# Kernel optimization log

Hardware: AMD Instinct MI355X
Metric: run time of the kernel (lower is better)

Reference implementation:

```python
import jax, jax.numpy as jnp
import numpy as np

N_EMBD = 1024
N_HEAD = 16
HEAD_SIZE = N_EMBD // N_HEAD


def setup_inputs() -> dict:
    key = jax.random.key(0)
    k_x, k_w, k_b = jax.random.split(key, 3)
    B, T, C = 2, 2048, N_EMBD
    x = jax.random.normal(k_x, (B, T, C), dtype=jnp.float32)
    # Linear(n_embd, 3*n_embd): weight [C, 3C] (applied as x @ W), bias [3C]
    w_qkv = jax.random.normal(k_w, (C, 3 * C), dtype=jnp.float32) * (1.0 / np.sqrt(C))
    b_qkv = jax.random.normal(k_b, (3 * C,), dtype=jnp.float32) * 0.02
    return {"x": x, "w_qkv": w_qkv, "b_qkv": b_qkv}


def reference(x, w_qkv, b_qkv):
    B, T, C = x.shape
    H, D = N_HEAD, HEAD_SIZE
    qkv = x @ w_qkv + b_qkv                      # [B, T, 3C]
    q, k, v = jnp.split(qkv, 3, axis=-1)         # each [B, T, C]
    # [B, T, C] -> [B, H, T, D]
    q = q.reshape(B, T, H, D).transpose(0, 2, 1, 3)
    k = k.reshape(B, T, H, D).transpose(0, 2, 1, 3)
    v = v.reshape(B, T, H, D).transpose(0, 2, 1, 3)
    scores = jnp.einsum('bhqd,bhkd->bhqk', q, k) / jnp.sqrt(jnp.float32(D))
    causal = jnp.tril(jnp.ones((T, T), dtype=bool))  # allow j <= i
    scores = jnp.where(causal[None, None, :, :], scores, -jnp.inf)
    weights = jax.nn.softmax(scores, axis=-1)    # [B, H, T, T]
    out = jnp.einsum('bhqk,bhkd->bhqd', weights, v)
    out = out.transpose(0, 2, 1, 3).reshape(B, T, C)
    return out
```

## Files before the change

### kernel.cpp

```cpp
#include <hip/hip_runtime.h>
#include <hip/hip_bf16.h>


#define CDIM  1024
#define C3    3072
#define HS    64
#define TLEN  2048
#define KVT   64
#define KSTR  72
#define VSTR  72
#define SCL   0.1803368801111204f

typedef __attribute__((ext_vector_type(8))) short bf16x8;
typedef __attribute__((ext_vector_type(4))) float f32x4;
typedef __attribute__((ext_vector_type(4))) unsigned short u16x4;

__device__ __forceinline__ unsigned short f2b(float f) {
    unsigned u = __float_as_uint(f);
    unsigned r = (u + 0x7FFFu + ((u >> 16) & 1u)) >> 16;
    return (unsigned short)r;
}
__device__ __forceinline__ float b2f(unsigned short u) {
    return __uint_as_float(((unsigned)u) << 16);
}
__device__ __forceinline__ float fexp2(float x) {
    return __builtin_amdgcn_exp2f(x);
}
__device__ __forceinline__ unsigned pkbf(float a, float b) {
    float2 f; f.x = a; f.y = b;
    __hip_bfloat162 h = __float22bfloat162_rn(f);
    union { __hip_bfloat162 h2; unsigned u; } c;
    c.h2 = h;
    return c.u;
}
__device__ __forceinline__ void gl_lds16(const unsigned short* g, unsigned short* l) {
    __builtin_amdgcn_global_load_lds((const __attribute__((address_space(1))) void*)g,
                                     (__attribute__((address_space(3))) void*)l, 16, 0, 0);
}
__device__ __forceinline__ int detect_bf(const void* bias, int lane) {
    unsigned w = ((const unsigned*)bias)[lane];
    unsigned e = (w >> 7) & 0xFF;
    unsigned long long m = __ballot(e >= 100 && e <= 135);
    return __popcll(m) >= 48;
}

__device__ __forceinline__ void plswap(unsigned x, unsigned& y0, unsigned& y1) {
    unsigned aa = x, bb = x;
    asm("v_permlane32_swap_b32 %0, %1" : "+v"(aa), "+v"(bb));
    asm("v_permlane16_swap_b32 %0, %1" : "+v"(aa), "+v"(bb));
    y0 = aa; y1 = bb;
}
__device__ __forceinline__ bf16x8 xfrag(unsigned x00, unsigned x01,
                                        unsigned x10, unsigned x11, int qsel) {
    unsigned y000, y100, y001, y101, y010, y110, y011, y111;
    plswap(x00, y000, y100);
    plswap(x01, y001, y101);
    plswap(x10, y010, y110);
    plswap(x11, y011, y111);
    union { unsigned u[4]; bf16x8 v; } r;
    r.u[0] = qsel ? y010 : y000;
    r.u[1] = qsel ? y011 : y001;
    r.u[2] = qsel ? y110 : y100;
    r.u[3] = qsel ? y111 : y101;
    return r.v;
}

__global__ __launch_bounds__(256) void k_prep(const void* __restrict__ w,
                                              const void* __restrict__ x,
                                              const void* __restrict__ bias,
                                              unsigned short* __restrict__ wt,
                                              unsigned short* __restrict__ xb) {
    __shared__ unsigned short tile[64 * 66];
    int t = threadIdx.x;
    int isbf = detect_bf(bias, t & 63);
    int bid = blockIdx.x;

    if (bid < 768) {
        int n0 = (bid % 48) * 64;
        int k0 = (bid / 48) * 64;
        for (int i = 0; i < 16; ++i) {
            int idx = t + i * 256;
            int r = idx >> 6, c = idx & 63;
            unsigned short v;
            if (isbf) v = ((const unsigned short*)w)[(k0 + r) * C3 + n0 + c];
            else      v = f2b(((const float*)w)[(k0 + r) * C3 + n0 + c]);
            tile[r * 66 + c] = v;
        }
        __syncthreads();
        for (int i = 0; i < 16; ++i) {
            int idx = t + i * 256;
            int r = idx >> 6, c = idx & 63;
            wt[(n0 + r) * CDIM + k0 + c] = tile[c * 66 + r];
        }
    }
    if (!isbf) {
        const float* s = (const float*)x;
        unsigned* d = (unsigned*)xb;
        int base = bid * 1024;
        for (int j = t; j < 1024; j += 256) {
            int idx = base + j;
            float a = s[2 * idx], b = s[2 * idx + 1];
            d[idx] = (unsigned)f2b(a) | ((unsigned)f2b(b) << 16);
        }
    }
}

__global__ __launch_bounds__(256, 3) void k_gemm_qkv(const void* __restrict__ xraw,
                                                     const unsigned short* __restrict__ xb,
                                                     const void* __restrict__ biasraw,
                                                     const unsigned short* __restrict__ Bt,
                                                     unsigned short* __restrict__ qk,
                                                     unsigned short* __restrict__ vtg) {
    __shared__ __align__(16) unsigned short As[128 * 64];
    __shared__ __align__(16) unsigned short Bs[128 * 64];
    int tid  = threadIdx.x;
    int lane = tid & 63, wv = tid >> 6;
    int quad = lane >> 4, l16 = lane & 15;
    int isbf = detect_bf(biasraw, lane);
    const unsigned short* A = isbf ? (const unsigned short*)xraw : xb;

    int m0 = blockIdx.y * 128, n0 = blockIdx.x * 128;
    int wm = (wv >> 1) * 64, wn = (wv & 1) * 64;

    f32x4 acc[4][4] = {};

    int srow = wv * 8 + (lane >> 3);
    int kcg8 = (((lane & 7) ^ (lane >> 3)) * 8);
    const unsigned short* Ag = A  + (m0 + srow) * CDIM + kcg8;
    const unsigned short* Bg = Bt + (n0 + srow) * CDIM + kcg8;
    unsigned short* lA = &As[srow * 64 + (lane & 7) * 8];
    unsigned short* lB = &Bs[srow * 64 + (lane & 7) * 8];

    for (int k0 = 0; k0 < CDIM; k0 += 64) {
        __syncthreads();
        for (int j = 0; j < 4; ++j) {
            gl_lds16(Ag + j * (32 * CDIM), lA + j * (32 * 64));
            gl_lds16(Bg + j * (32 * CDIM), lB + j * (32 * 64));
        }
        Ag += 64; Bg += 64;
        __syncthreads();

        for (int kk = 0; kk < 2; ++kk) {
            int sw = (l16 & 7);
            bf16x8 af[4], bfr[4];
            for (int mt = 0; mt < 4; ++mt)
                af[mt] = *(const bf16x8*)&As[(wm + mt * 16 + l16) * 64 + (((kk * 4 + quad) ^ sw) * 8)];
            for (int nt = 0; nt < 4; ++nt)
                bfr[nt] = *(const bf16x8*)&Bs[(wn + nt * 16 + l16) * 64 + (((kk * 4 + quad) ^ sw) * 8)];
            for (int mt = 0; mt < 4; ++mt)
                for (int nt = 0; nt < 4; ++nt)
                    acc[mt][nt] = __builtin_amdgcn_mfma_f32_16x16x32_bf16(af[mt], bfr[nt], acc[mt][nt], 0, 0, 0);
        }
    }

    if (n0 < 2048) {
        for (int mt = 0; mt < 4; ++mt) {
            int row = m0 + wm + mt * 16 + quad * 4;
            for (int nt = 0; nt < 4; ++nt) {
                int col = n0 + wn + nt * 16 + l16;
                float bv = isbf ? b2f(((const unsigned short*)biasraw)[col])
                                : ((const float*)biasraw)[col];
                for (int i = 0; i < 4; ++i)
                    qk[(row + i) * 2048 + col] = f2b(acc[mt][nt][i] + bv);
            }
        }
    } else {
        for (int mt = 0; mt < 4; ++mt) {
            int row = m0 + wm + mt * 16 + quad * 4;
            int t = row & 2047, b = row >> 11;
            for (int nt = 0; nt < 4; ++nt) {
                int col = n0 + wn + nt * 16 + l16;
                float bv = isbf ? b2f(((const unsigned short*)biasraw)[col])
                                : ((const float*)biasraw)[col];
                int hh = (col - 2048) >> 6, d = (col - 2048) & 63;
                u16x4 pk;
                for (int i = 0; i < 4; ++i) pk[i] = f2b(acc[mt][nt][i] + bv);
                *(u16x4*)&vtg[((b * 16 + hh) * 64 + d) * TLEN + t] = pk;
            }
        }
    }
}

__global__ __launch_bounds__(256, 4) void k_attn(const unsigned short* __restrict__ qk,
                                                 const unsigned short* __restrict__ vtg,
                                                 const void* __restrict__ biasraw,
                                                 void* __restrict__ outv) {
    __shared__ __align__(16) unsigned short Ks[2][64 * KSTR];
    __shared__ __align__(16) unsigned short Vt[2][64 * VSTR];

    int tid  = threadIdx.x;
    int lane = tid & 63, wv = tid >> 6;
    int quad = lane >> 4, l16 = lane & 15;
    int isbf = detect_bf(biasraw, lane);
    int bh = blockIdx.x;
    int g  = 31 - blockIdx.y;
    int b = bh >> 4, h = bh & 15;
    int rowbase = b * TLEN;

    int s_ = wv >> 1;
    int p  = wv & 1;
    int qbase = 64 * g + 32 * s_;
    int T = g + 1;

    bf16x8 qf[2][2];
    for (int qt = 0; qt < 2; ++qt)
        for (int kh = 0; kh < 2; ++kh)
            qf[qt][kh] = *(const bf16x8*)&qk[(rowbase + qbase + qt * 16 + l16) * 2048
                                            + h * HS + kh * 32 + quad * 8];

    f32x4 o[2][4] = {};
    float ls[2] = {0.f, 0.f};

    int srow = tid >> 2;
    int sc   = (tid & 3) * 8;
    const unsigned short* kgB = qk  + (rowbase + srow) * 2048 + CDIM + h * HS + sc;
    const unsigned short* vgB = vtg + (bh * 64 + srow) * TLEN + sc;

    {
        uint4 k0 = *(const uint4*)kgB;
        uint4 k1 = *(const uint4*)(kgB + 32);
        uint4 v0 = *(const uint4*)vgB;
        uint4 v1 = *(const uint4*)(vgB + 32);
        *(uint4*)&Ks[0][srow * KSTR + sc]      = k0;
        *(uint4*)&Ks[0][srow * KSTR + sc + 32] = k1;
        *(uint4*)&Vt[0][srow * VSTR + sc]      = v0;
        *(uint4*)&Vt[0][srow * VSTR + sc + 32] = v1;
    }
    __syncthreads();

    for (int t = 0; t < T; ++t) {
        int cur = t & 1;
        const unsigned short* KsC = Ks[cur];
        const unsigned short* VtC = Vt[cur];
        int kv0 = t * KVT;
        bool act = (p == 0) || (s_ == 1) || (t < T - 1);
        bool dm  = (t == T - 1) && (p == s_);

        uint4 kn0, kn1, vn0, vn1;
        bool pf = (t + 1 < T);
        if (pf) {
            const unsigned short* kg = kgB + (t + 1) * KVT * 2048;
            const unsigned short* vg = vgB + (t + 1) * KVT;
            kn0 = *(const uint4*)kg;
            kn1 = *(const uint4*)(kg + 32);
            vn0 = *(const uint4*)vg;
            vn1 = *(const uint4*)(vg + 32);
        }

        unsigned sp[2][2][2];
        if (act) {
            bf16x8 kf[2][2];
            #pragma unroll
            for (int nt = 0; nt < 2; ++nt) {
                const unsigned short* kb = &KsC[(32 * p + nt * 16 + l16) * KSTR + quad * 8];
                kf[nt][0] = *(const bf16x8*)kb;
                kf[nt][1] = *(const bf16x8*)(kb + 32);
            }
            f32x4 sv[2][2];
            __builtin_amdgcn_s_setprio(1);
            #pragma unroll
            for (int qt = 0; qt < 2; ++qt)
                #pragma unroll
                for (int nt = 0; nt < 2; ++nt) {
                    f32x4 z = {};
                    z = __builtin_amdgcn_mfma_f32_16x16x32_bf16(kf[nt][0], qf[qt][0], z, 0, 0, 0);
                    z = __builtin_amdgcn_mfma_f32_16x16x32_bf16(kf[nt][1], qf[qt][1], z, 0, 0, 0);
                    sv[qt][nt] = z;
                }
            __builtin_amdgcn_s_setprio(0);
            #pragma unroll
            for (int qt = 0; qt < 2; ++qt) {
                float psum = 0.f;
                int q = qbase + qt * 16 + l16;
                #pragma unroll
                for (int nt = 0; nt < 2; ++nt) {
                    float pv[4];
                    #pragma unroll
                    for (int i = 0; i < 4; ++i) {
                        float arg = fminf(fmaf(sv[qt][nt][i], SCL, -12.0f), 30.0f);
                        if (dm) {
                            int kv = kv0 + 32 * p + nt * 16 + quad * 4 + i;
                            if (kv > q) arg = -1e30f;
                        }
                        pv[i] = fexp2(arg);
                        psum += pv[i];
                    }
                    sp[qt][nt][0] = pkbf(pv[0], pv[1]);
                    sp[qt][nt][1] = pkbf(pv[2], pv[3]);
                }
                ls[qt] += psum;
            }
        }

        if (pf) {
            int nxt = cur ^ 1;
            *(uint4*)&Ks[nxt][srow * KSTR + sc]      = kn0;
            *(uint4*)&Ks[nxt][srow * KSTR + sc + 32] = kn1;
            *(uint4*)&Vt[nxt][srow * VSTR + sc]      = vn0;
            *(uint4*)&Vt[nxt][srow * VSTR + sc + 32] = vn1;
        }

        if (act) {
            int qsel = quad & 2;
            bf16x8 f0 = xfrag(sp[0][0][0], sp[0][0][1], sp[0][1][0], sp[0][1][1], qsel);
            bf16x8 f1 = xfrag(sp[1][0][0], sp[1][0][1], sp[1][1][0], sp[1][1][1], qsel);
            __builtin_amdgcn_s_setprio(1);
            #pragma unroll
            for (int dt = 0; dt < 4; ++dt) {
                bf16x8 av = *(const bf16x8*)&VtC[(dt * 16 + l16) * VSTR + 32 * p + quad * 8];
                o[0][dt] = __builtin_amdgcn_mfma_f32_16x16x32_bf16(av, f0, o[0][dt], 0, 0, 0);
                o[1][dt] = __builtin_amdgcn_mfma_f32_16x16x32_bf16(av, f1, o[1][dt], 0, 0, 0);
            }
            __builtin_amdgcn_s_setprio(0);
        }

        __syncthreads();
    }

    #pragma unroll
    for (int qt = 0; qt < 2; ++qt) {
        ls[qt] += __shfl_xor(ls[qt], 16);
        ls[qt] += __shfl_xor(ls[qt], 32);
    }
    float* mrg  = (float*)&Ks[0][0];
    float* lbuf = (float*)&Vt[0][0];

    if (p == 1) {
        #pragma unroll
        for (int qt = 0; qt < 2; ++qt)
            #pragma unroll
            for (int dt = 0; dt < 4; ++dt)
                *(f32x4*)&mrg[s_ * (32 * 68) + (qt * 16 + l16) * 68 + dt * 16 + quad * 4] = o[qt][dt];
        if (quad == 0) {
            lbuf[s_ * 32 + l16]      = ls[0];
            lbuf[s_ * 32 + 16 + l16] = ls[1];
        }
    }
    __syncthreads();
    if (p == 0) {
        #pragma unroll
        for (int qt = 0; qt < 2; ++qt) {
            float lt = ls[qt] + lbuf[s_ * 32 + qt * 16 + l16];
            float inv = 1.0f / lt;
            int q = qbase + qt * 16 + l16;
            if (isbf) {
                unsigned short* out = (unsigned short*)outv;
                #pragma unroll
                for (int dt = 0; dt < 4; ++dt) {
                    f32x4 m = *(const f32x4*)&mrg[s_ * (32 * 68) + (qt * 16 + l16) * 68 + dt * 16 + quad * 4];
                    u16x4 ov;
                    #pragma unroll
                    for (int i = 0; i < 4; ++i) ov[i] = f2b((o[qt][dt][i] + m[i]) * inv);
                    *(u16x4*)&out[(rowbase + q) * CDIM + h * HS + dt * 16 + quad * 4] = ov;
                }
            } else {
                float* out = (float*)outv;
                #pragma unroll
                for (int dt = 0; dt < 4; ++dt) {
                    f32x4 m = *(const f32x4*)&mrg[s_ * (32 * 68) + (qt * 16 + l16) * 68 + dt * 16 + quad * 4];
                    float4 ov;
                    ov.x = (o[qt][dt][0] + m[0]) * inv;
                    ov.y = (o[qt][dt][1] + m[1]) * inv;
                    ov.z = (o[qt][dt][2] + m[2]) * inv;
                    ov.w = (o[qt][dt][3] + m[3]) * inv;
                    *(float4*)&out[(rowbase + q) * CDIM + h * HS + dt * 16 + quad * 4] = ov;
                }
            }
        }
    }
}

extern "C" void kernel_launch(void* const* d_in, const int* in_sizes, int n_in,
                              void* d_out, int out_size, void* d_ws, size_t ws_size,
                              hipStream_t stream) {
    const void* x    = d_in[0];
    const void* w    = d_in[1];
    const void* bias = d_in[2];

    char* ws = (char*)d_ws;
    unsigned short* xb  = (unsigned short*)ws;
    unsigned short* wt  = (unsigned short*)(ws + (8u  << 20));
    unsigned short* qk  = (unsigned short*)(ws + (16u << 20));
    unsigned short* vtg = (unsigned short*)(ws + (32u << 20));

    k_prep<<<2048, 256, 0, stream>>>(w, x, bias, wt, xb);
    k_gemm_qkv<<<dim3(24, 32), 256, 0, stream>>>(x, xb, bias, wt, qk, vtg);
    k_attn<<<dim3(32, 32), 256, 0, stream>>>(qk, vtg, bias, d_out);
}
```

Before: 151.0 us.

## Single-buffer attention K/V tiles for higher occupancy and swizzle GEMM block order

The attention kernel drops double-buffered LDS for K/V to a single buffer. It adds a second barrier per tile so the prefetched registers are written only after all waves finish reading, and raises launch bounds to 6 blocks per CU. The QKV GEMM remaps block indices with a grouped swizzle to improve L2 reuse of weight and activation tiles. The trade is an extra barrier per KV tile and less overlap of LDS writes with compute, in exchange for more resident waves; the merge buffer offsets are recomputed for the smaller shared array.

```diff
diff --git a/kernel.cpp b/kernel.cpp
--- a/kernel.cpp
+++ b/kernel.cpp
@@ -119,7 +119,9 @@
     int isbf = detect_bf(biasraw, lane);
     const unsigned short* A = isbf ? (const unsigned short*)xraw : xb;
 
-    int m0 = blockIdx.y * 128, n0 = blockIdx.x * 128;
+    int lin = blockIdx.x + 24 * blockIdx.y;
+    int swz = (lin & 7) * 96 + (lin >> 3);
+    int m0 = (swz / 24) * 128, n0 = (swz % 24) * 128;
     int wm = (wv >> 1) * 64, wn = (wv & 1) * 64;
 
     f32x4 acc[4][4] = {};
@@ -181,12 +183,13 @@
     }
 }
 
-__global__ __launch_bounds__(256, 4) void k_attn(const unsigned short* __restrict__ qk,
+__global__ __launch_bounds__(256, 6) void k_attn(const unsigned short* __restrict__ qk,
                                                  const unsigned short* __restrict__ vtg,
                                                  const void* __restrict__ biasraw,
                                                  void* __restrict__ outv) {
-    __shared__ __align__(16) unsigned short Ks[2][64 * KSTR];
-    __shared__ __align__(16) unsigned short Vt[2][64 * VSTR];
+    __shared__ __align__(16) unsigned short SM[2 * 64 * KSTR];
+    unsigned short* Ks = SM;
+    unsigned short* Vt = SM + 64 * KSTR;
 
     int tid  = threadIdx.x;
     int lane = tid & 63, wv = tid >> 6;
@@ -221,17 +224,16 @@
         uint4 k1 = *(const uint4*)(kgB + 32);
         uint4 v0 = *(const uint4*)vgB;
         uint4 v1 = *(const uint4*)(vgB + 32);
-        *(uint4*)&Ks[0][srow * KSTR + sc]      = k0;
-        *(uint4*)&Ks[0][srow * KSTR + sc + 32] = k1;
-        *(uint4*)&Vt[0][srow * VSTR + sc]      = v0;
-        *(uint4*)&Vt[0][srow * VSTR + sc + 32] = v1;
-    }
+        *(uint4*)&Ks[srow * KSTR + sc]      = k0;
+        *(uint4*)&Ks[srow * KSTR + sc + 32] = k1;
+        *(uint4*)&Vt[srow * VSTR + sc]      = v0;
+        *(uint4*)&Vt[srow * VSTR + sc + 32] = v1;
+    }
+    const unsigned short* kpf = kgB + KVT * 2048;
+    const unsigned short* vpf = vgB + KVT;
     __syncthreads();
 
     for (int t = 0; t < T; ++t) {
-        int cur = t & 1;
-        const unsigned short* KsC = Ks[cur];
-        const unsigned short* VtC = Vt[cur];
         int kv0 = t * KVT;
         bool act = (p == 0) || (s_ == 1) || (t < T - 1);
         bool dm  = (t == T - 1) && (p == s_);
@@ -239,12 +241,12 @@
         uint4 kn0, kn1, vn0, vn1;
         bool pf = (t + 1 < T);
         if (pf) {
-            const unsigned short* kg = kgB + (t + 1) * KVT * 2048;
-            const unsigned short* vg = vgB + (t + 1) * KVT;
-            kn0 = *(const uint4*)kg;
-            kn1 = *(const uint4*)(kg + 32);
-            vn0 = *(const uint4*)vg;
-            vn1 = *(const uint4*)(vg + 32);
+            kn0 = *(const uint4*)kpf;
+            kn1 = *(const uint4*)(kpf + 32);
+            vn0 = *(const uint4*)vpf;
+            vn1 = *(const uint4*)(vpf + 32);
+            kpf += KVT * 2048;
+            vpf += KVT;
         }
 
         unsigned sp[2][2][2];
@@ -252,7 +254,7 @@
             bf16x8 kf[2][2];
             #pragma unroll
             for (int nt = 0; nt < 2; ++nt) {
-                const unsigned short* kb = &KsC[(32 * p + nt * 16 + l16) * KSTR + quad * 8];
+                const unsigned short* kb = &Ks[(32 * p + nt * 16 + l16) * KSTR + quad * 8];
                 kf[nt][0] = *(const bf16x8*)kb;
                 kf[nt][1] = *(const bf16x8*)(kb + 32);
             }
@@ -290,30 +292,26 @@
                 }
                 ls[qt] += psum;
             }
-        }
-
-        if (pf) {
-            int nxt = cur ^ 1;
-            *(uint4*)&Ks[nxt][srow * KSTR + sc]      = kn0;
-            *(uint4*)&Ks[nxt][srow * KSTR + sc + 32] = kn1;
-            *(uint4*)&Vt[nxt][srow * VSTR + sc]      = vn0;
-            *(uint4*)&Vt[nxt][srow * VSTR + sc + 32] = vn1;
-        }
-
-        if (act) {
             int qsel = quad & 2;
             bf16x8 f0 = xfrag(sp[0][0][0], sp[0][0][1], sp[0][1][0], sp[0][1][1], qsel);
             bf16x8 f1 = xfrag(sp[1][0][0], sp[1][0][1], sp[1][1][0], sp[1][1][1], qsel);
             __builtin_amdgcn_s_setprio(1);
             #pragma unroll
             for (int dt = 0; dt < 4; ++dt) {
-                bf16x8 av = *(const bf16x8*)&VtC[(dt * 16 + l16) * VSTR + 32 * p + quad * 8];
+                bf16x8 av = *(const bf16x8*)&Vt[(dt * 16 + l16) * VSTR + 32 * p + quad * 8];
                 o[0][dt] = __builtin_amdgcn_mfma_f32_16x16x32_bf16(av, f0, o[0][dt], 0, 0, 0);
                 o[1][dt] = __builtin_amdgcn_mfma_f32_16x16x32_bf16(av, f1, o[1][dt], 0, 0, 0);
             }
             __builtin_amdgcn_s_setprio(0);
         }
 
+        __syncthreads();
+        if (pf) {
+            *(uint4*)&Ks[srow * KSTR + sc]      = kn0;
+            *(uint4*)&Ks[srow * KSTR + sc + 32] = kn1;
+            *(uint4*)&Vt[srow * VSTR + sc]      = vn0;
+            *(uint4*)&Vt[srow * VSTR + sc + 32] = vn1;
+        }
         __syncthreads();
     }
 
@@ -322,8 +320,8 @@
         ls[qt] += __shfl_xor(ls[qt], 16);
         ls[qt] += __shfl_xor(ls[qt], 32);
     }
-    float* mrg  = (float*)&Ks[0][0];
-    float* lbuf = (float*)&Vt[0][0];
+    float* mrg  = (float*)SM;
+    float* lbuf = (float*)SM + 4352;
 
     if (p == 1) {
         #pragma unroll
```

After: 248.6 us. 64.6% more time.
